# Kernel optimization log

Measured on AMD Instinct MI355X. Metric: run time of the kernel, lower is better.

The kernel has to match this reference:

```python
import jax, jax.numpy as jnp
import numpy as np

N_NODES = 100000
N_EDGES = 1600000
IN_DIM = 256
OUT_DIM = 128


def setup_inputs() -> dict:
    key = jax.random.key(0)
    ks = jax.random.split(key, 8)
    x = jax.random.normal(ks[0], (N_NODES, IN_DIM), dtype=jnp.float32)
    # glorot-ish init scaling
    W = jax.random.normal(ks[1], (IN_DIM, OUT_DIM), dtype=jnp.float32) * (6.0 / (IN_DIM + OUT_DIM)) ** 0.5
    fsW = jax.random.normal(ks[2], (IN_DIM, OUT_DIM), dtype=jnp.float32) * (6.0 / (IN_DIM + OUT_DIM)) ** 0.5
    f_weights = jax.random.normal(ks[3], (2 * OUT_DIM, 1), dtype=jnp.float32) * (6.0 / (2 * OUT_DIM + 1)) ** 0.5
    f_bias = jnp.zeros((1,), dtype=jnp.float32)
    # degrees in [1, 64], strictly positive so pow(deg, -p) is finite
    dia_adj = jax.random.uniform(ks[4], (N_NODES,), dtype=jnp.float32) * 63.0 + 1.0
    row = jax.random.randint(ks[5], (N_EDGES,), 0, N_NODES, dtype=jnp.int32)
    col = jax.random.randint(ks[6], (N_EDGES,), 0, N_NODES, dtype=jnp.int32)
    return {"x": x, "W": W, "fsW": fsW, "f_weights": f_weights,
            "f_bias": f_bias, "dia_adj": dia_adj, "row": row, "col": col}


def reference(x, W, fsW, f_weights, f_bias, dia_adj, row, col):
    # pre_sup = x @ weights_, fpre_sup = x @ fs_weights  (dropout=0, dense inputs)
    pre_sup = x @ W                 # [N, out]
    fpre_sup = x @ fsW              # [N, out]
    d = W.shape[1]
    # concat([vi, vj]) @ f_weights == vi @ f_weights[:d] + vj @ f_weights[d:]
    wi, wj = f_weights[:d], f_weights[d:]
    score = jax.nn.sigmoid(fpre_sup[row] @ wi + fpre_sup[col] @ wj + f_bias)  # [E, 1]
    # degree-power normalization: (deg_i * deg_j) ** (-sigmoid_score)
    deg_vivj = (dia_adj[row] * dia_adj[col])[:, None]                         # [E, 1]
    vals = jnp.power(deg_vivj, -score)[:, 0]                                  # [E]
    # sparse matmul: out[r] += vals_e * pre_sup[c] for each edge e=(r,c)
    msg = vals[:, None] * pre_sup[col]                                        # [E, out]
    out = jax.ops.segment_sum(msg, row, num_segments=x.shape[0])              # [N, out]
    return jax.nn.relu(out)
```

## Files before the change

### kernel.cpp

```cpp
#include <hip/hip_runtime.h>

#define N_NODES 100000
#define N_EDGES 1600000
#define IN_DIM 256
#define OUT_DIM 128
#define BROWS 100
#define NBK 1000
#define PBLK 128
#define EPB 12500

typedef __attribute__((ext_vector_type(4))) float f32x4;
typedef __attribute__((ext_vector_type(8))) short s16x8;

__device__ inline unsigned short f2bf(float f) {
    union { float f; unsigned int u; } a; a.f = f;
    unsigned int r = a.u + 0x7fffu + ((a.u >> 16) & 1u);
    return (unsigned short)(r >> 16);
}
__device__ inline float bf2f(unsigned short h) {
    union { unsigned int u; float f; } a; a.u = ((unsigned int)h) << 16;
    return a.f;
}

__global__ __launch_bounds__(256) void kprep(
        const float* __restrict__ fsW, const float* __restrict__ fw,
        const float* __restrict__ W, const int* __restrict__ row,
        float* __restrict__ u, float* __restrict__ v,
        unsigned short* __restrict__ wt, int* __restrict__ hist_t) {
    __shared__ int h[NBK];
    __shared__ float wi[128], wj[128];
    const int t = threadIdx.x, blk = blockIdx.x;
    if (blk < PBLK) {
        wt[blk * 256 + t] = f2bf(W[(size_t)t * 128 + blk]);
        for (int b = t; b < NBK; b += 256) h[b] = 0;
        __syncthreads();
        const int e0 = blk * EPB;
        for (int i = t; i < EPB; i += 256)
            atomicAdd(&h[row[e0 + i] / BROWS], 1);
        __syncthreads();
        for (int b = t; b < NBK; b += 256)
            hist_t[b * PBLK + blk] = h[b];
    } else {
        if (t < 128) wi[t] = fw[t]; else wj[t - 128] = fw[t];
        __syncthreads();
        const float* rowp = fsW + (size_t)t * OUT_DIM;
        float su = 0.f, sv = 0.f;
        for (int d = 0; d < 128; d += 4) {
            float4 a = *(const float4*)(rowp + d);
            su += a.x * wi[d] + a.y * wi[d + 1] + a.z * wi[d + 2] + a.w * wi[d + 3];
            sv += a.x * wj[d] + a.y * wj[d + 1] + a.z * wj[d + 2] + a.w * wj[d + 3];
        }
        u[t] = su; v[t] = sv;
    }
}

__global__ __launch_bounds__(1024) void kbscan(const int* __restrict__ hist_t,
                                               int* __restrict__ bpre) {
    __shared__ int s[1024];
    const int t = threadIdx.x;
    int v = 0;
    if (t < NBK) {
        const int4* hp = (const int4*)(hist_t + t * PBLK);
#pragma unroll 4
        for (int k = 0; k < PBLK / 4; ++k) {
            int4 a = hp[k];
            v += a.x + a.y + a.z + a.w;
        }
    }
    s[t] = v;
    __syncthreads();
    for (int off = 1; off < 1024; off <<= 1) {
        int nv = (t >= off) ? s[t - off] : 0;
        __syncthreads();
        s[t] += nv;
        __syncthreads();
    }
    if (t < NBK) bpre[t] = s[t] - v;
    if (t == 1023) bpre[NBK] = s[1023];
}

__global__ __launch_bounds__(128) void koff(const int* __restrict__ hist_t,
                                            const int* __restrict__ bpre,
                                            int* __restrict__ off) {
    const int b = blockIdx.x, t = threadIdx.x;
    const int lane = t & 63, w = t >> 6;
    int v = hist_t[b * PBLK + t];
    int s = v;
#pragma unroll
    for (int o = 1; o < 64; o <<= 1) { int tt = __shfl_up(s, o); if (lane >= o) s += tt; }
    __shared__ int ws2[2];
    if (lane == 63) ws2[w] = s;
    __syncthreads();
    int base = (w == 1) ? ws2[0] : 0;
    off[b * PBLK + t] = bpre[b] + base + (s - v);
}

__global__ __launch_bounds__(256) void gpart(
        const float* __restrict__ x, const unsigned short* __restrict__ wt,
        const float* __restrict__ u, const float* __restrict__ v,
        unsigned short* __restrict__ psb, float* __restrict__ si, float* __restrict__ sj,
        const int* __restrict__ row, const int* __restrict__ col,
        const int* __restrict__ off, unsigned int* __restrict__ part) {
    __shared__ unsigned short xa[64 * 136];

    const int t = threadIdx.x;

    if (blockIdx.x < PBLK) {
        int* cur = (int*)xa;
        const int blk = blockIdx.x;
        for (int b = t; b < NBK; b += 256) cur[b] = off[b * PBLK + blk];
        __syncthreads();
        const int e0 = blk * EPB;
        for (int i = t; i < EPB; i += 256) {
            int r = row[e0 + i], c = col[e0 + i];
            int b = r / BROWS;
            int rl = r - b * BROWS;
            int pos = atomicAdd(&cur[b], 1);
            part[pos] = ((unsigned)rl << 17) | (unsigned)c;
        }
        return;
    }

    const int wave = t >> 6, lane = t & 63;
    const int l15 = lane & 15, lhi = lane >> 4;
    const int rw = t >> 2, quad = t & 3;
    const int brow = (blockIdx.x - PBLK) * 64;
    const int gnode = brow + rw;
    const bool valid = gnode < N_NODES;

    f32x4 acc[4][2];
#pragma unroll
    for (int mi = 0; mi < 4; ++mi)
#pragma unroll
        for (int ni = 0; ni < 2; ++ni) acc[mi][ni] = (f32x4){0.f, 0.f, 0.f, 0.f};
    float su = 0.f, sv = 0.f;

    const float* xp = x + (size_t)gnode * IN_DIM + quad * 16;
    float4 xr[4];
#pragma unroll
    for (int i = 0; i < 4; ++i) xr[i] = make_float4(0.f, 0.f, 0.f, 0.f);
    if (valid) {
#pragma unroll
        for (int i = 0; i < 4; ++i) xr[i] = ((const float4*)xp)[i];
    }

#pragma unroll
    for (int ph = 0; ph < 4; ++ph) {
        {
            const float* up = u + ph * 64 + quad * 16;
            const float* vp = v + ph * 64 + quad * 16;
            float4 uu0 = ((const float4*)up)[0], uu1 = ((const float4*)up)[1];
            float4 uu2 = ((const float4*)up)[2], uu3 = ((const float4*)up)[3];
            float4 vv0 = ((const float4*)vp)[0], vv1 = ((const float4*)vp)[1];
            float4 vv2 = ((const float4*)vp)[2], vv3 = ((const float4*)vp)[3];
            su = fmaf(xr[0].x, uu0.x, su); su = fmaf(xr[0].y, uu0.y, su);
            su = fmaf(xr[0].z, uu0.z, su); su = fmaf(xr[0].w, uu0.w, su);
            su = fmaf(xr[1].x, uu1.x, su); su = fmaf(xr[1].y, uu1.y, su);
            su = fmaf(xr[1].z, uu1.z, su); su = fmaf(xr[1].w, uu1.w, su);
            su = fmaf(xr[2].x, uu2.x, su); su = fmaf(xr[2].y, uu2.y, su);
            su = fmaf(xr[2].z, uu2.z, su); su = fmaf(xr[2].w, uu2.w, su);
            su = fmaf(xr[3].x, uu3.x, su); su = fmaf(xr[3].y, uu3.y, su);
            su = fmaf(xr[3].z, uu3.z, su); su = fmaf(xr[3].w, uu3.w, su);
            sv = fmaf(xr[0].x, vv0.x, sv); sv = fmaf(xr[0].y, vv0.y, sv);
            sv = fmaf(xr[0].z, vv0.z, sv); sv = fmaf(xr[0].w, vv0.w, sv);
            sv = fmaf(xr[1].x, vv1.x, sv); sv = fmaf(xr[1].y, vv1.y, sv);
            sv = fmaf(xr[1].z, vv1.z, sv); sv = fmaf(xr[1].w, vv1.w, sv);
            sv = fmaf(xr[2].x, vv2.x, sv); sv = fmaf(xr[2].y, vv2.y, sv);
            sv = fmaf(xr[2].z, vv2.z, sv); sv = fmaf(xr[2].w, vv2.w, sv);
            sv = fmaf(xr[3].x, vv3.x, sv); sv = fmaf(xr[3].y, vv3.y, sv);
            sv = fmaf(xr[3].z, vv3.z, sv); sv = fmaf(xr[3].w, vv3.w, sv);
            union { unsigned short h[16]; uint4 q[2]; } pk;
#pragma unroll
            for (int i = 0; i < 4; ++i) {
                pk.h[i * 4 + 0] = f2bf(xr[i].x); pk.h[i * 4 + 1] = f2bf(xr[i].y);
                pk.h[i * 4 + 2] = f2bf(xr[i].z); pk.h[i * 4 + 3] = f2bf(xr[i].w);
            }
            *(uint4*)&xa[rw * 72 + quad * 16]     = pk.q[0];
            *(uint4*)&xa[rw * 72 + quad * 16 + 8] = pk.q[1];
        }
        if (ph < 3) {
            const float* xpn = xp + (ph + 1) * 64;
            if (valid) {
#pragma unroll
                for (int i = 0; i < 4; ++i) xr[i] = ((const float4*)xpn)[i];
            }
        }
        asm volatile("s_waitcnt lgkmcnt(0)" ::: "memory");
        __builtin_amdgcn_s_barrier();
        {
            const unsigned short* wb0 = wt + (size_t)(wave * 32 + l15) * IN_DIM + ph * 64 + lhi * 8;
            s16x8 bfr[2][2];
#pragma unroll
            for (int ks = 0; ks < 2; ++ks) {
                bfr[ks][0] = *(const s16x8*)(wb0 + ks * 32);
                bfr[ks][1] = *(const s16x8*)(wb0 + (size_t)16 * IN_DIM + ks * 32);
            }
#pragma unroll
            for (int ks = 0; ks < 2; ++ks) {
                const int k0 = ks * 32 + lhi * 8;
                s16x8 afr[4];
#pragma unroll
                for (int mi = 0; mi < 4; ++mi)
                    afr[mi] = *(const s16x8*)&xa[(mi * 16 + l15) * 72 + k0];
#pragma unroll
                for (int mi = 0; mi < 4; ++mi)
#pragma unroll
                    for (int ni = 0; ni < 2; ++ni)
                        acc[mi][ni] = __builtin_amdgcn_mfma_f32_16x16x32_bf16(
                            afr[mi], bfr[ks][ni], acc[mi][ni], 0, 0, 0);
            }
        }
        __builtin_amdgcn_s_barrier();
    }

    su += __shfl_xor(su, 1); su += __shfl_xor(su, 2);
    sv += __shfl_xor(sv, 1); sv += __shfl_xor(sv, 2);
    if (quad == 0 && valid) { si[gnode] = su; sj[gnode] = sv; }

    unsigned short* cl = xa;
#pragma unroll
    for (int mi = 0; mi < 4; ++mi)
#pragma unroll
        for (int ni = 0; ni < 2; ++ni) {
            const int colb = wave * 32 + ni * 16 + l15;
#pragma unroll
            for (int j = 0; j < 4; ++j)
                cl[(mi * 16 + lhi * 4 + j) * 128 + colb] = f2bf(acc[mi][ni][j]);
        }
    __syncthreads();
    {
        const int rl = t >> 2;
        const int cb = (t & 3) * 32;
        if (brow + rl < N_NODES) {
            const uint4* src = (const uint4*)&cl[rl * 128 + cb];
            uint4* dst = (uint4*)&psb[(size_t)(brow + rl) * OUT_DIM + cb];
            dst[0] = src[0]; dst[1] = src[1]; dst[2] = src[2]; dst[3] = src[3];
        }
    }
}

__global__ __launch_bounds__(256) void kpart2(const unsigned int* __restrict__ part,
                                              const int* __restrict__ bpre,
                                              const float* __restrict__ si,
                                              const float* __restrict__ sj,
                                              const float* __restrict__ dia,
                                              const float* __restrict__ fb,
                                              int2* __restrict__ epack,
                                              int* __restrict__ offs,
                                              int* __restrict__ deg) {
    __shared__ int cnt[BROWS];
    __shared__ int cur[BROWS];
    __shared__ float sil[BROWS], dial[BROWS];
    __shared__ int wtot[4];
    const int b = blockIdx.x, t = threadIdx.x;
    const int rbase = b * BROWS;
    if (t < BROWS) {
        cnt[t] = 0;
        sil[t] = si[rbase + t];
        dial[t] = dia[rbase + t];
    }
    __syncthreads();
    const int bstart = bpre[b], bend = bpre[b + 1];
    for (int e = bstart + t; e < bend; e += 256)
        atomicAdd(&cnt[part[e] >> 17], 1);
    __syncthreads();
    {
        int vv = (t < BROWS) ? cnt[t] : 0;
        int lane = t & 63, w = t >> 6;
        int s = vv;
#pragma unroll
        for (int o = 1; o < 64; o <<= 1) { int tt = __shfl_up(s, o); if (lane >= o) s += tt; }
        if (lane == 63) wtot[w] = s;
        __syncthreads();
        int base = 0;
        for (int k = 0; k < w; ++k) base += wtot[k];
        int excl = base + s - vv;
        if (t < BROWS) {
            cur[t] = bstart + excl;
            offs[rbase + t] = bstart + excl;
            deg[rbase + t] = vv;
        }
    }
    __syncthreads();
    const float fbv = fb[0];
    for (int e = bstart + t; e < bend; e += 256) {
        unsigned pk = part[e];
        int rl = (int)(pk >> 17);
        int c = (int)(pk & 0x1FFFFu);
        float tval = sil[rl] + sj[c] + fbv;
        float sg = 1.f / (1.f + expf(-tval));
        float l2 = log2f(dial[rl] * dia[c]);
        float val = exp2f(-sg * l2);
        int pos = atomicAdd(&cur[rl], 1);
        epack[pos] = make_int2(c, __float_as_int(val));
    }
}

__global__ __launch_bounds__(256) void kgather(
        const int* __restrict__ offs, const int* __restrict__ deg,
        const int2* __restrict__ epack,
        const unsigned short* __restrict__ psb, float* __restrict__ out) {
    int lane = threadIdx.x & 31;
    int node = blockIdx.x * 8 + (threadIdx.x >> 5);
    if (node >= N_NODES) return;
    int start = offs[node], d = deg[node];
    const int2* ep = epack + start;
    float a0 = 0.f, a1 = 0.f, a2 = 0.f, a3 = 0.f;
    int k = 0;
    for (; k + 8 <= d; k += 8) {
        int2 e0 = ep[k],     e1 = ep[k + 1], e2 = ep[k + 2], e3 = ep[k + 3];
        int2 e4 = ep[k + 4], e5 = ep[k + 5], e6 = ep[k + 6], e7 = ep[k + 7];
        ushort4 p0 = *(const ushort4*)&psb[(size_t)e0.x * OUT_DIM + lane * 4];
        ushort4 p1 = *(const ushort4*)&psb[(size_t)e1.x * OUT_DIM + lane * 4];
        ushort4 p2 = *(const ushort4*)&psb[(size_t)e2.x * OUT_DIM + lane * 4];
        ushort4 p3 = *(const ushort4*)&psb[(size_t)e3.x * OUT_DIM + lane * 4];
        ushort4 p4 = *(const ushort4*)&psb[(size_t)e4.x * OUT_DIM + lane * 4];
        ushort4 p5 = *(const ushort4*)&psb[(size_t)e5.x * OUT_DIM + lane * 4];
        ushort4 p6 = *(const ushort4*)&psb[(size_t)e6.x * OUT_DIM + lane * 4];
        ushort4 p7 = *(const ushort4*)&psb[(size_t)e7.x * OUT_DIM + lane * 4];
        float v0 = __int_as_float(e0.y), v1 = __int_as_float(e1.y);
        float v2 = __int_as_float(e2.y), v3 = __int_as_float(e3.y);
        float v4 = __int_as_float(e4.y), v5 = __int_as_float(e5.y);
        float v6 = __int_as_float(e6.y), v7 = __int_as_float(e7.y);
        a0 = fmaf(v0, bf2f(p0.x), a0); a1 = fmaf(v0, bf2f(p0.y), a1);
        a2 = fmaf(v0, bf2f(p0.z), a2); a3 = fmaf(v0, bf2f(p0.w), a3);
        a0 = fmaf(v1, bf2f(p1.x), a0); a1 = fmaf(v1, bf2f(p1.y), a1);
        a2 = fmaf(v1, bf2f(p1.z), a2); a3 = fmaf(v1, bf2f(p1.w), a3);
        a0 = fmaf(v2, bf2f(p2.x), a0); a1 = fmaf(v2, bf2f(p2.y), a1);
        a2 = fmaf(v2, bf2f(p2.z), a2); a3 = fmaf(v2, bf2f(p2.w), a3);
        a0 = fmaf(v3, bf2f(p3.x), a0); a1 = fmaf(v3, bf2f(p3.y), a1);
        a2 = fmaf(v3, bf2f(p3.z), a2); a3 = fmaf(v3, bf2f(p3.w), a3);
        a0 = fmaf(v4, bf2f(p4.x), a0); a1 = fmaf(v4, bf2f(p4.y), a1);
        a2 = fmaf(v4, bf2f(p4.z), a2); a3 = fmaf(v4, bf2f(p4.w), a3);
        a0 = fmaf(v5, bf2f(p5.x), a0); a1 = fmaf(v5, bf2f(p5.y), a1);
        a2 = fmaf(v5, bf2f(p5.z), a2); a3 = fmaf(v5, bf2f(p5.w), a3);
        a0 = fmaf(v6, bf2f(p6.x), a0); a1 = fmaf(v6, bf2f(p6.y), a1);
        a2 = fmaf(v6, bf2f(p6.z), a2); a3 = fmaf(v6, bf2f(p6.w), a3);
        a0 = fmaf(v7, bf2f(p7.x), a0); a1 = fmaf(v7, bf2f(p7.y), a1);
        a2 = fmaf(v7, bf2f(p7.z), a2); a3 = fmaf(v7, bf2f(p7.w), a3);
    }
    for (; k < d; ++k) {
        int2 e0 = ep[k];
        float v0 = __int_as_float(e0.y);
        ushort4 p0 = *(const ushort4*)&psb[(size_t)e0.x * OUT_DIM + lane * 4];
        a0 = fmaf(v0, bf2f(p0.x), a0);
        a1 = fmaf(v0, bf2f(p0.y), a1);
        a2 = fmaf(v0, bf2f(p0.z), a2);
        a3 = fmaf(v0, bf2f(p0.w), a3);
    }
    float4 o;
    o.x = fmaxf(a0, 0.f); o.y = fmaxf(a1, 0.f);
    o.z = fmaxf(a2, 0.f); o.w = fmaxf(a3, 0.f);
    *(float4*)&out[(size_t)node * OUT_DIM + lane * 4] = o;
}

extern "C" void kernel_launch(void* const* d_in, const int* in_sizes, int n_in,
                              void* d_out, int out_size, void* d_ws, size_t ws_size,
                              hipStream_t stream) {
    const float* x   = (const float*)d_in[0];
    const float* W   = (const float*)d_in[1];
    const float* fsW = (const float*)d_in[2];
    const float* fw  = (const float*)d_in[3];
    const float* fb  = (const float*)d_in[4];
    const float* dia = (const float*)d_in[5];
    const int*   row = (const int*)d_in[6];
    const int*   col = (const int*)d_in[7];
    float* out = (float*)d_out;

    char* p = (char*)d_ws;
    auto alloc = [&](size_t bytes) -> char* {
        char* r = p; p += (bytes + 255) & ~(size_t)255; return r;
    };
    float* u      = (float*)alloc(256 * 4);
    float* v      = (float*)alloc(256 * 4);
    unsigned short* wtb = (unsigned short*)alloc((size_t)128 * 256 * 2);
    float* si     = (float*)alloc((size_t)N_NODES * 4);
    float* sj     = (float*)alloc((size_t)N_NODES * 4);
    int*   deg    = (int*)alloc((size_t)N_NODES * 4);
    int*   offs   = (int*)alloc((size_t)N_NODES * 4);
    unsigned short* psb = (unsigned short*)alloc((size_t)N_NODES * OUT_DIM * 2);
    int*   hist_t = (int*)alloc((size_t)NBK * PBLK * 4);
    int*   bpre   = (int*)alloc((size_t)(NBK + 1) * 4);
    int*   off    = (int*)alloc((size_t)NBK * PBLK * 4);
    unsigned int* part = (unsigned int*)alloc((size_t)N_EDGES * 4);
    int2*  epack  = (int2*)alloc((size_t)N_EDGES * 8);

    kprep<<<PBLK + 1, 256, 0, stream>>>(fsW, fw, W, row, u, v, wtb, hist_t);
    kbscan<<<1, 1024, 0, stream>>>(hist_t, bpre);
    koff<<<NBK, PBLK, 0, stream>>>(hist_t, bpre, off);
    gpart<<<PBLK + (N_NODES + 63) / 64, 256, 0, stream>>>(
        x, wtb, u, v, psb, si, sj, row, col, off, part);
    kpart2<<<NBK, 256, 0, stream>>>(part, bpre, si, sj, dia, fb, epack, offs, deg);
    kgather<<<N_NODES / 8, 256, 0, stream>>>(offs, deg, epack, psb, out);
}
```

Before: 186.4 us.

## Fuse edge-value computation and gather aggregation into one per-bucket kernel

Merges kpart2 and kgather into a single kernel. Each 100-row bucket block computes the edge values, scatters them into epack, syncs, then aggregates its own rows directly, using offsets and counts kept in shared memory. This drops a kernel launch and the global offs/deg round trip, and the epack reads likely hit cache. The cost is only 1000 blocks of 256 threads doing the gather instead of 12500, so there is less parallelism for hiding gather latency, and per-block work becomes serialized.

```diff
diff --git a/kernel.cpp b/kernel.cpp
--- a/kernel.cpp
+++ b/kernel.cpp
@@ -239,17 +239,15 @@
     }
 }
 
-__global__ __launch_bounds__(256) void kpart2(const unsigned int* __restrict__ part,
-                                              const int* __restrict__ bpre,
-                                              const float* __restrict__ si,
-                                              const float* __restrict__ sj,
-                                              const float* __restrict__ dia,
-                                              const float* __restrict__ fb,
-                                              int2* __restrict__ epack,
-                                              int* __restrict__ offs,
-                                              int* __restrict__ deg) {
+__global__ __launch_bounds__(256) void kedge(
+        const unsigned int* __restrict__ part, const int* __restrict__ bpre,
+        const float* __restrict__ si, const float* __restrict__ sj,
+        const float* __restrict__ dia, const float* __restrict__ fb,
+        int2* __restrict__ epack, const unsigned short* __restrict__ psb,
+        float* __restrict__ out) {
     __shared__ int cnt[BROWS];
     __shared__ int cur[BROWS];
+    __shared__ int st[BROWS];
     __shared__ float sil[BROWS], dial[BROWS];
     __shared__ int wtot[4];
     const int b = blockIdx.x, t = threadIdx.x;
@@ -277,8 +275,7 @@
         int excl = base + s - vv;
         if (t < BROWS) {
             cur[t] = bstart + excl;
-            offs[rbase + t] = bstart + excl;
-            deg[rbase + t] = vv;
+            st[t] = bstart + excl;
         }
     }
     __syncthreads();
@@ -294,64 +291,60 @@
         int pos = atomicAdd(&cur[rl], 1);
         epack[pos] = make_int2(c, __float_as_int(val));
     }
-}
-
-__global__ __launch_bounds__(256) void kgather(
-        const int* __restrict__ offs, const int* __restrict__ deg,
-        const int2* __restrict__ epack,
-        const unsigned short* __restrict__ psb, float* __restrict__ out) {
-    int lane = threadIdx.x & 31;
-    int node = blockIdx.x * 8 + (threadIdx.x >> 5);
-    if (node >= N_NODES) return;
-    int start = offs[node], d = deg[node];
-    const int2* ep = epack + start;
-    float a0 = 0.f, a1 = 0.f, a2 = 0.f, a3 = 0.f;
-    int k = 0;
-    for (; k + 8 <= d; k += 8) {
-        int2 e0 = ep[k],     e1 = ep[k + 1], e2 = ep[k + 2], e3 = ep[k + 3];
-        int2 e4 = ep[k + 4], e5 = ep[k + 5], e6 = ep[k + 6], e7 = ep[k + 7];
-        ushort4 p0 = *(const ushort4*)&psb[(size_t)e0.x * OUT_DIM + lane * 4];
-        ushort4 p1 = *(const ushort4*)&psb[(size_t)e1.x * OUT_DIM + lane * 4];
-        ushort4 p2 = *(const ushort4*)&psb[(size_t)e2.x * OUT_DIM + lane * 4];
-        ushort4 p3 = *(const ushort4*)&psb[(size_t)e3.x * OUT_DIM + lane * 4];
-        ushort4 p4 = *(const ushort4*)&psb[(size_t)e4.x * OUT_DIM + lane * 4];
-        ushort4 p5 = *(const ushort4*)&psb[(size_t)e5.x * OUT_DIM + lane * 4];
-        ushort4 p6 = *(const ushort4*)&psb[(size_t)e6.x * OUT_DIM + lane * 4];
-        ushort4 p7 = *(const ushort4*)&psb[(size_t)e7.x * OUT_DIM + lane * 4];
-        float v0 = __int_as_float(e0.y), v1 = __int_as_float(e1.y);
-        float v2 = __int_as_float(e2.y), v3 = __int_as_float(e3.y);
-        float v4 = __int_as_float(e4.y), v5 = __int_as_float(e5.y);
-        float v6 = __int_as_float(e6.y), v7 = __int_as_float(e7.y);
-        a0 = fmaf(v0, bf2f(p0.x), a0); a1 = fmaf(v0, bf2f(p0.y), a1);
-        a2 = fmaf(v0, bf2f(p0.z), a2); a3 = fmaf(v0, bf2f(p0.w), a3);
-        a0 = fmaf(v1, bf2f(p1.x), a0); a1 = fmaf(v1, bf2f(p1.y), a1);
-        a2 = fmaf(v1, bf2f(p1.z), a2); a3 = fmaf(v1, bf2f(p1.w), a3);
-        a0 = fmaf(v2, bf2f(p2.x), a0); a1 = fmaf(v2, bf2f(p2.y), a1);
-        a2 = fmaf(v2, bf2f(p2.z), a2); a3 = fmaf(v2, bf2f(p2.w), a3);
-        a0 = fmaf(v3, bf2f(p3.x), a0); a1 = fmaf(v3, bf2f(p3.y), a1);
-        a2 = fmaf(v3, bf2f(p3.z), a2); a3 = fmaf(v3, bf2f(p3.w), a3);
-        a0 = fmaf(v4, bf2f(p4.x), a0); a1 = fmaf(v4, bf2f(p4.y), a1);
-        a2 = fmaf(v4, bf2f(p4.z), a2); a3 = fmaf(v4, bf2f(p4.w), a3);
-        a0 = fmaf(v5, bf2f(p5.x), a0); a1 = fmaf(v5, bf2f(p5.y), a1);
-        a2 = fmaf(v5, bf2f(p5.z), a2); a3 = fmaf(v5, bf2f(p5.w), a3);
-        a0 = fmaf(v6, bf2f(p6.x), a0); a1 = fmaf(v6, bf2f(p6.y), a1);
-        a2 = fmaf(v6, bf2f(p6.z), a2); a3 = fmaf(v6, bf2f(p6.w), a3);
-        a0 = fmaf(v7, bf2f(p7.x), a0); a1 = fmaf(v7, bf2f(p7.y), a1);
-        a2 = fmaf(v7, bf2f(p7.z), a2); a3 = fmaf(v7, bf2f(p7.w), a3);
-    }
-    for (; k < d; ++k) {
-        int2 e0 = ep[k];
-        float v0 = __int_as_float(e0.y);
-        ushort4 p0 = *(const ushort4*)&psb[(size_t)e0.x * OUT_DIM + lane * 4];
-        a0 = fmaf(v0, bf2f(p0.x), a0);
-        a1 = fmaf(v0, bf2f(p0.y), a1);
-        a2 = fmaf(v0, bf2f(p0.z), a2);
-        a3 = fmaf(v0, bf2f(p0.w), a3);
-    }
-    float4 o;
-    o.x = fmaxf(a0, 0.f); o.y = fmaxf(a1, 0.f);
-    o.z = fmaxf(a2, 0.f); o.w = fmaxf(a3, 0.f);
-    *(float4*)&out[(size_t)node * OUT_DIM + lane * 4] = o;
+    __syncthreads();
+
+    const int lane = t & 31, grp = t >> 5;
+    for (int rl = grp; rl < BROWS; rl += 8) {
+        const int start = st[rl], d = cnt[rl];
+        const int2* ep = epack + start;
+        float a0 = 0.f, a1 = 0.f, a2 = 0.f, a3 = 0.f;
+        int k = 0;
+        for (; k + 8 <= d; k += 8) {
+            int2 e0 = ep[k],     e1 = ep[k + 1], e2 = ep[k + 2], e3 = ep[k + 3];
+            int2 e4 = ep[k + 4], e5 = ep[k + 5], e6 = ep[k + 6], e7 = ep[k + 7];
+            ushort4 p0 = *(const ushort4*)&psb[(size_t)e0.x * OUT_DIM + lane * 4];
+            ushort4 p1 = *(const ushort4*)&psb[(size_t)e1.x * OUT_DIM + lane * 4];
+            ushort4 p2 = *(const ushort4*)&psb[(size_t)e2.x * OUT_DIM + lane * 4];
+            ushort4 p3 = *(const ushort4*)&psb[(size_t)e3.x * OUT_DIM + lane * 4];
+            ushort4 p4 = *(const ushort4*)&psb[(size_t)e4.x * OUT_DIM + lane * 4];
+            ushort4 p5 = *(const ushort4*)&psb[(size_t)e5.x * OUT_DIM + lane * 4];
+            ushort4 p6 = *(const ushort4*)&psb[(size_t)e6.x * OUT_DIM + lane * 4];
+            ushort4 p7 = *(const ushort4*)&psb[(size_t)e7.x * OUT_DIM + lane * 4];
+            float v0 = __int_as_float(e0.y), v1 = __int_as_float(e1.y);
+            float v2 = __int_as_float(e2.y), v3 = __int_as_float(e3.y);
+            float v4 = __int_as_float(e4.y), v5 = __int_as_float(e5.y);
+            float v6 = __int_as_float(e6.y), v7 = __int_as_float(e7.y);
+            a0 = fmaf(v0, bf2f(p0.x), a0); a1 = fmaf(v0, bf2f(p0.y), a1);
+            a2 = fmaf(v0, bf2f(p0.z), a2); a3 = fmaf(v0, bf2f(p0.w), a3);
+            a0 = fmaf(v1, bf2f(p1.x), a0); a1 = fmaf(v1, bf2f(p1.y), a1);
+            a2 = fmaf(v1, bf2f(p1.z), a2); a3 = fmaf(v1, bf2f(p1.w), a3);
+            a0 = fmaf(v2, bf2f(p2.x), a0); a1 = fmaf(v2, bf2f(p2.y), a1);
+            a2 = fmaf(v2, bf2f(p2.z), a2); a3 = fmaf(v2, bf2f(p2.w), a3);
+            a0 = fmaf(v3, bf2f(p3.x), a0); a1 = fmaf(v3, bf2f(p3.y), a1);
+            a2 = fmaf(v3, bf2f(p3.z), a2); a3 = fmaf(v3, bf2f(p3.w), a3);
+            a0 = fmaf(v4, bf2f(p4.x), a0); a1 = fmaf(v4, bf2f(p4.y), a1);
+            a2 = fmaf(v4, bf2f(p4.z), a2); a3 = fmaf(v4, bf2f(p4.w), a3);
+            a0 = fmaf(v5, bf2f(p5.x), a0); a1 = fmaf(v5, bf2f(p5.y), a1);
+            a2 = fmaf(v5, bf2f(p5.z), a2); a3 = fmaf(v5, bf2f(p5.w), a3);
+            a0 = fmaf(v6, bf2f(p6.x), a0); a1 = fmaf(v6, bf2f(p6.y), a1);
+            a2 = fmaf(v6, bf2f(p6.z), a2); a3 = fmaf(v6, bf2f(p6.w), a3);
+            a0 = fmaf(v7, bf2f(p7.x), a0); a1 = fmaf(v7, bf2f(p7.y), a1);
+            a2 = fmaf(v7, bf2f(p7.z), a2); a3 = fmaf(v7, bf2f(p7.w), a3);
+        }
+        for (; k < d; ++k) {
+            int2 e0 = ep[k];
+            float v0 = __int_as_float(e0.y);
+            ushort4 p0 = *(const ushort4*)&psb[(size_t)e0.x * OUT_DIM + lane * 4];
+            a0 = fmaf(v0, bf2f(p0.x), a0);
+            a1 = fmaf(v0, bf2f(p0.y), a1);
+            a2 = fmaf(v0, bf2f(p0.z), a2);
+            a3 = fmaf(v0, bf2f(p0.w), a3);
+        }
+        float4 o;
+        o.x = fmaxf(a0, 0.f); o.y = fmaxf(a1, 0.f);
+        o.z = fmaxf(a2, 0.f); o.w = fmaxf(a3, 0.f);
+        *(float4*)&out[(size_t)(rbase + rl) * OUT_DIM + lane * 4] = o;
+    }
 }
 
 extern "C" void kernel_launch(void* const* d_in, const int* in_sizes, int n_in,
@@ -376,8 +369,6 @@
     unsigned short* wtb = (unsigned short*)alloc((size_t)128 * 256 * 2);
     float* si     = (float*)alloc((size_t)N_NODES * 4);
     float* sj     = (float*)alloc((size_t)N_NODES * 4);
-    int*   deg    = (int*)alloc((size_t)N_NODES * 4);
-    int*   offs   = (int*)alloc((size_t)N_NODES * 4);
     unsigned short* psb = (unsigned short*)alloc((size_t)N_NODES * OUT_DIM * 2);
     int*   hist_t = (int*)alloc((size_t)NBK * PBLK * 4);
     int*   bpre   = (int*)alloc((size_t)(NBK + 1) * 4);
@@ -390,6 +381,5 @@
     koff<<<NBK, PBLK, 0, stream>>>(hist_t, bpre, off);
     gpart<<<PBLK + (N_NODES + 63) / 64, 256, 0, stream>>>(
         x, wtb, u, v, psb, si, sj, row, col, off, part);
-    kpart2<<<NBK, 256, 0, stream>>>(part, bpre, si, sj, dia, fb, epack, offs, deg);
-    kgather<<<N_NODES / 8, 256, 0, stream>>>(offs, deg, epack, psb, out);
-}
+    kedge<<<NBK, 256, 0, stream>>>(part, bpre, si, sj, dia, fb, epack, psb, out);
+}
```

After: 199.0 us. 1.07x slower.

## Stage x tiles via direct global-to-LDS loads with XOR swizzle, convert to bf16 at fragment read

Applied to the files above, without the earlier changes.

Each x tile is now loaded straight into shared memory with global_load_lds in fp32, using an XOR swizzle, instead of passing through registers, being converted to bf16 and stored. The bf16 conversion moves to the MFMA fragment reads through a packed convert instruction, and the u/v dot products read x from LDS after the MFMAs. The goal is to cut register traffic and VALU work in the staging path. In exchange the register prefetch of the next phase is gone, so each phase now waits on its load behind a full barrier, LDS traffic doubles, and conversion is repeated per fragment.

```diff
diff --git a/kernel.cpp b/kernel.cpp
--- a/kernel.cpp
+++ b/kernel.cpp
@@ -20,6 +20,11 @@
 __device__ inline float bf2f(unsigned short h) {
     union { unsigned int u; float f; } a; a.u = ((unsigned int)h) << 16;
     return a.f;
+}
+__device__ inline void gload16(const void* g, void* l) {
+    __builtin_amdgcn_global_load_lds(
+        (const __attribute__((address_space(1))) void*)g,
+        (__attribute__((address_space(3))) void*)l, 16, 0, 0);
 }
 
 __global__ __launch_bounds__(256) void kprep(
@@ -101,12 +106,12 @@
         unsigned short* __restrict__ psb, float* __restrict__ si, float* __restrict__ sj,
         const int* __restrict__ row, const int* __restrict__ col,
         const int* __restrict__ off, unsigned int* __restrict__ part) {
-    __shared__ unsigned short xa[64 * 136];
+    __shared__ char ldsraw[16640];
 
     const int t = threadIdx.x;
 
     if (blockIdx.x < PBLK) {
-        int* cur = (int*)xa;
+        int* cur = (int*)ldsraw;
         const int blk = blockIdx.x;
         for (int b = t; b < NBK; b += 256) cur[b] = off[b * PBLK + blk];
         __syncthreads();
@@ -135,58 +140,19 @@
         for (int ni = 0; ni < 2; ++ni) acc[mi][ni] = (f32x4){0.f, 0.f, 0.f, 0.f};
     float su = 0.f, sv = 0.f;
 
-    const float* xp = x + (size_t)gnode * IN_DIM + quad * 16;
-    float4 xr[4];
-#pragma unroll
-    for (int i = 0; i < 4; ++i) xr[i] = make_float4(0.f, 0.f, 0.f, 0.f);
-    if (valid) {
-#pragma unroll
-        for (int i = 0; i < 4; ++i) xr[i] = ((const float4*)xp)[i];
-    }
-
 #pragma unroll
     for (int ph = 0; ph < 4; ++ph) {
-        {
-            const float* up = u + ph * 64 + quad * 16;
-            const float* vp = v + ph * 64 + quad * 16;
-            float4 uu0 = ((const float4*)up)[0], uu1 = ((const float4*)up)[1];
-            float4 uu2 = ((const float4*)up)[2], uu3 = ((const float4*)up)[3];
-            float4 vv0 = ((const float4*)vp)[0], vv1 = ((const float4*)vp)[1];
-            float4 vv2 = ((const float4*)vp)[2], vv3 = ((const float4*)vp)[3];
-            su = fmaf(xr[0].x, uu0.x, su); su = fmaf(xr[0].y, uu0.y, su);
-            su = fmaf(xr[0].z, uu0.z, su); su = fmaf(xr[0].w, uu0.w, su);
-            su = fmaf(xr[1].x, uu1.x, su); su = fmaf(xr[1].y, uu1.y, su);
-            su = fmaf(xr[1].z, uu1.z, su); su = fmaf(xr[1].w, uu1.w, su);
-            su = fmaf(xr[2].x, uu2.x, su); su = fmaf(xr[2].y, uu2.y, su);
-            su = fmaf(xr[2].z, uu2.z, su); su = fmaf(xr[2].w, uu2.w, su);
-            su = fmaf(xr[3].x, uu3.x, su); su = fmaf(xr[3].y, uu3.y, su);
-            su = fmaf(xr[3].z, uu3.z, su); su = fmaf(xr[3].w, uu3.w, su);
-            sv = fmaf(xr[0].x, vv0.x, sv); sv = fmaf(xr[0].y, vv0.y, sv);
-            sv = fmaf(xr[0].z, vv0.z, sv); sv = fmaf(xr[0].w, vv0.w, sv);
-            sv = fmaf(xr[1].x, vv1.x, sv); sv = fmaf(xr[1].y, vv1.y, sv);
-            sv = fmaf(xr[1].z, vv1.z, sv); sv = fmaf(xr[1].w, vv1.w, sv);
-            sv = fmaf(xr[2].x, vv2.x, sv); sv = fmaf(xr[2].y, vv2.y, sv);
-            sv = fmaf(xr[2].z, vv2.z, sv); sv = fmaf(xr[2].w, vv2.w, sv);
-            sv = fmaf(xr[3].x, vv3.x, sv); sv = fmaf(xr[3].y, vv3.y, sv);
-            sv = fmaf(xr[3].z, vv3.z, sv); sv = fmaf(xr[3].w, vv3.w, sv);
-            union { unsigned short h[16]; uint4 q[2]; } pk;
-#pragma unroll
-            for (int i = 0; i < 4; ++i) {
-                pk.h[i * 4 + 0] = f2bf(xr[i].x); pk.h[i * 4 + 1] = f2bf(xr[i].y);
-                pk.h[i * 4 + 2] = f2bf(xr[i].z); pk.h[i * 4 + 3] = f2bf(xr[i].w);
-            }
-            *(uint4*)&xa[rw * 72 + quad * 16]     = pk.q[0];
-            *(uint4*)&xa[rw * 72 + quad * 16 + 8] = pk.q[1];
-        }
-        if (ph < 3) {
-            const float* xpn = xp + (ph + 1) * 64;
-            if (valid) {
-#pragma unroll
-                for (int i = 0; i < 4; ++i) xr[i] = ((const float4*)xpn)[i];
-            }
-        }
-        asm volatile("s_waitcnt lgkmcnt(0)" ::: "memory");
-        __builtin_amdgcn_s_barrier();
+#pragma unroll
+        for (int i = 0; i < 4; ++i) {
+            int lo = i * 4096 + t * 16;
+            int q  = lo ^ (((lo >> 8) & 7) << 4);
+            int grow = brow + (q >> 8);
+            if (grow >= N_NODES) grow = N_NODES - 1;
+            gload16((const char*)x + (size_t)grow * 1024 + ph * 256 + (q & 255),
+                    ldsraw + lo);
+        }
+        __syncthreads();
+
         {
             const unsigned short* wb0 = wt + (size_t)(wave * 32 + l15) * IN_DIM + ph * 64 + lhi * 8;
             s16x8 bfr[2][2];
@@ -197,11 +163,21 @@
             }
 #pragma unroll
             for (int ks = 0; ks < 2; ++ks) {
-                const int k0 = ks * 32 + lhi * 8;
                 s16x8 afr[4];
 #pragma unroll
-                for (int mi = 0; mi < 4; ++mi)
-                    afr[mi] = *(const s16x8*)&xa[(mi * 16 + l15) * 72 + k0];
+                for (int mi = 0; mi < 4; ++mi) {
+                    const int r = mi * 16 + l15;
+                    const int sw = (r & 7) << 4;
+                    const int b0 = r * 256 + ks * 128 + lhi * 32;
+                    float4 f0 = *(const float4*)(ldsraw + (b0 ^ sw));
+                    float4 f1 = *(const float4*)(ldsraw + ((b0 + 16) ^ sw));
+                    union { unsigned int w[4]; s16x8 s; } cv;
+                    asm("v_cvt_pk_bf16_f32 %0, %1, %2" : "=v"(cv.w[0]) : "v"(f0.x), "v"(f0.y));
+                    asm("v_cvt_pk_bf16_f32 %0, %1, %2" : "=v"(cv.w[1]) : "v"(f0.z), "v"(f0.w));
+                    asm("v_cvt_pk_bf16_f32 %0, %1, %2" : "=v"(cv.w[2]) : "v"(f1.x), "v"(f1.y));
+                    asm("v_cvt_pk_bf16_f32 %0, %1, %2" : "=v"(cv.w[3]) : "v"(f1.z), "v"(f1.w));
+                    afr[mi] = cv.s;
+                }
 #pragma unroll
                 for (int mi = 0; mi < 4; ++mi)
 #pragma unroll
@@ -210,14 +186,31 @@
                             afr[mi], bfr[ks][ni], acc[mi][ni], 0, 0, 0);
             }
         }
-        __builtin_amdgcn_s_barrier();
+
+        {
+            const float* up = u + ph * 64 + quad * 16;
+            const float* vp = v + ph * 64 + quad * 16;
+            const int rb_ = rw * 256 + quad * 64;
+            const int sw = (rw & 7) << 4;
+#pragma unroll
+            for (int c = 0; c < 4; ++c) {
+                float4 a = *(const float4*)(ldsraw + ((rb_ + c * 16) ^ sw));
+                float4 uu = ((const float4*)up)[c];
+                float4 vv = ((const float4*)vp)[c];
+                su = fmaf(a.x, uu.x, su); su = fmaf(a.y, uu.y, su);
+                su = fmaf(a.z, uu.z, su); su = fmaf(a.w, uu.w, su);
+                sv = fmaf(a.x, vv.x, sv); sv = fmaf(a.y, vv.y, sv);
+                sv = fmaf(a.z, vv.z, sv); sv = fmaf(a.w, vv.w, sv);
+            }
+        }
+        __syncthreads();
     }
 
     su += __shfl_xor(su, 1); su += __shfl_xor(su, 2);
     sv += __shfl_xor(sv, 1); sv += __shfl_xor(sv, 2);
     if (quad == 0 && valid) { si[gnode] = su; sj[gnode] = sv; }
 
-    unsigned short* cl = xa;
+    unsigned short* cl = (unsigned short*)ldsraw;
 #pragma unroll
     for (int mi = 0; mi < 4; ++mi)
 #pragma unroll
```

After: 174.4 us. 6.4% less time.
